# Kernel tuning notes

Hardware: AMD Instinct MI355X
Metric: run time of the kernel (lower is better)

## Reference

```python
import jax, jax.numpy as jnp
import numpy as np

N_NODES = 100000
N_EDGES = 3200000
STATE_DIM = 128
HIDDEN = 256
ACTION_DIM = 64
BN_EPS = 1e-5


def setup_inputs() -> dict:
    key = jax.random.key(0)
    ks = jax.random.split(key, 12)
    feat = jax.random.normal(ks[0], (N_NODES, STATE_DIM), dtype=jnp.float32)
    src = jax.random.randint(ks[1], (N_EDGES,), 0, N_NODES, dtype=jnp.int64) if jax.config.jax_enable_x64 else jax.random.randint(ks[1], (N_EDGES,), 0, N_NODES).astype(jnp.int32)
    dst = jax.random.randint(ks[2], (N_EDGES,), 0, N_NODES).astype(src.dtype)
    def glorot(k, shape):
        lim = np.sqrt(6.0 / (shape[0] + shape[1]))
        return jax.random.uniform(k, shape, jnp.float32, -lim, lim)
    W1 = glorot(ks[3], (STATE_DIM, HIDDEN)); b1 = jnp.zeros((HIDDEN,), jnp.float32)
    W2 = glorot(ks[4], (HIDDEN, HIDDEN));   b2 = jnp.zeros((HIDDEN,), jnp.float32)
    g1 = jnp.ones((HIDDEN,), jnp.float32);  be1 = jnp.zeros((HIDDEN,), jnp.float32)
    g2 = jnp.ones((HIDDEN,), jnp.float32);  be2 = jnp.zeros((HIDDEN,), jnp.float32)
    Wa = glorot(ks[5], (HIDDEN, ACTION_DIM)); ba = jnp.zeros((ACTION_DIM,), jnp.float32)
    Wv = glorot(ks[6], (HIDDEN, 1));          bv = jnp.zeros((1,), jnp.float32)
    return {"feat": feat, "src": src, "dst": dst, "W1": W1, "b1": b1, "g1": g1, "be1": be1,
            "W2": W2, "b2": b2, "g2": g2, "be2": be2, "Wa": Wa, "ba": ba, "Wv": Wv, "bv": bv}


def _graph_conv(x, src, dst, dnorm_out, dnorm_in, W, b):
    # DGL GraphConv, norm='both': scale by out-deg^{-1/2} at src, sum-aggregate at dst,
    # scale by in-deg^{-1/2}, then linear.
    m = x * dnorm_out[:, None]                     # [N, F]
    agg = jax.ops.segment_sum(m[src], dst, num_segments=N_NODES)  # SpMM
    h = agg * dnorm_in[:, None]
    return h @ W + b


def _bn_relu(x, gamma, beta):
    mu = x.mean(axis=0)
    var = x.var(axis=0)  # biased, matches torch BN training normalization
    return jax.nn.relu((x - mu) * jax.lax.rsqrt(var + BN_EPS) * gamma + beta)


def reference(feat, src, dst, W1, b1, g1, be1, W2, b2, g2, be2, Wa, ba, Wv, bv):
    ones = jnp.ones((src.shape[0],), feat.dtype)
    deg_out = jax.ops.segment_sum(ones, src, num_segments=N_NODES)
    deg_in = jax.ops.segment_sum(ones, dst, num_segments=N_NODES)
    dnorm_out = jax.lax.rsqrt(jnp.clip(deg_out, 1.0))
    dnorm_in = jax.lax.rsqrt(jnp.clip(deg_in, 1.0))
    h = _bn_relu(_graph_conv(feat, src, dst, dnorm_out, dnorm_in, W1, b1), g1, be1)
    h = _bn_relu(_graph_conv(h, src, dst, dnorm_out, dnorm_in, W2, b2), g2, be2)
    adv = h @ Wa + ba                              # [N, A]
    val = h @ Wv + bv                              # [N, 1]
    Q = val + (adv - adv.mean(axis=1, keepdims=True))
    return Q
```

## Files before the change

kernel.cpp:

```cpp
#include <hip/hip_runtime.h>
#include <hip/hip_bf16.h>

#define NN 100000
#define NE 3200000
#define HID 256
#define SDIM 128
#define ADIM 64
#define BN_EPS 1e-5f

#define BSH 9
#define NB 196
#define EPB 16384
#define NAB 196

typedef __attribute__((ext_vector_type(8))) short short8;
typedef __attribute__((ext_vector_type(4))) float f32x4;

__device__ __forceinline__ void atomAdd(float* p, float v) { unsafeAtomicAdd(p, v); }
__device__ __forceinline__ float bf2f(ushort u) {
    union { unsigned i; float f; } c; c.i = ((unsigned)u) << 16; return c.f;
}
__device__ __forceinline__ ushort f2bf(float x) {
    __hip_bfloat16 h = __float2bfloat16(x);
    return *reinterpret_cast<ushort*>(&h);
}

__device__ __forceinline__ unsigned wave_excl_scan(unsigned t, int lane) {
    unsigned p = t;
    #pragma unroll
    for (int d = 1; d < 64; d <<= 1) {
        unsigned q = __shfl_up(p, d);
        if (lane >= d) p += q;
    }
    return p - t;
}

__global__ __launch_bounds__(1024)
void k_hist(const int* __restrict__ src, const int* __restrict__ dst,
            unsigned* __restrict__ gh_d, unsigned* __restrict__ gh_s, int E) {
    __shared__ unsigned hd[NB], hs[NB];
    int tid = threadIdx.x;
    if (tid < NB) { hd[tid] = 0; hs[tid] = 0; }
    __syncthreads();
    int base = blockIdx.x * EPB;
    int cnt = min(EPB, E - base);
    for (int i = tid; i < cnt; i += 1024) {
        atomicAdd(&hd[dst[base + i] >> BSH], 1u);
        atomicAdd(&hs[src[base + i] >> BSH], 1u);
    }
    __syncthreads();
    if (tid < NB) {
        if (hd[tid]) atomicAdd(&gh_d[tid * 16], hd[tid]);
        if (hs[tid]) atomicAdd(&gh_s[tid * 16], hs[tid]);
    }
}

__global__ __launch_bounds__(256)
void k_scan_b(const unsigned* __restrict__ gh_d, const unsigned* __restrict__ gh_s,
              unsigned* __restrict__ gcur_d, unsigned* __restrict__ gcur_s,
              unsigned* __restrict__ bbase_d, unsigned* __restrict__ bbase_s,
              int* __restrict__ row_ptr) {
    __shared__ unsigned v[256];
    int t = threadIdx.x;
    unsigned x = (t < NB) ? gh_d[t * 16] : 0;
    v[t] = x; __syncthreads();
    for (int off = 1; off < 256; off <<= 1) {
        unsigned a = (t >= off) ? v[t - off] : 0;
        __syncthreads(); v[t] += a; __syncthreads();
    }
    if (t < NB) { bbase_d[t] = v[t] - x; gcur_d[t * 16] = v[t] - x; }
    if (t == 255) { bbase_d[NB] = v[255]; row_ptr[NN] = (int)v[255]; }
    __syncthreads();
    unsigned y = (t < NB) ? gh_s[t * 16] : 0;
    v[t] = y; __syncthreads();
    for (int off = 1; off < 256; off <<= 1) {
        unsigned a = (t >= off) ? v[t - off] : 0;
        __syncthreads(); v[t] += a; __syncthreads();
    }
    if (t < NB) { bbase_s[t] = v[t] - y; gcur_s[t * 16] = v[t] - y; }
    if (t == 255) bbase_s[NB] = v[255];
}

__global__ __launch_bounds__(1024)
void k_part(const int* __restrict__ src, const int* __restrict__ dst,
            unsigned* __restrict__ gcur_d, unsigned* __restrict__ gcur_s,
            unsigned* __restrict__ outd, ushort* __restrict__ outs, int E) {
    __shared__ unsigned hd[NB], hs[NB], ld_[NB], ls_[NB], cd[NB], cs[NB], bd[NB], bs[NB];
    __shared__ unsigned stage_d[EPB];
    __shared__ ushort stage_s[EPB];
    __shared__ unsigned char sbd[EPB], sbs[EPB];
    const int tid = threadIdx.x;
    const int base = blockIdx.x * EPB;
    const int cnt = min(EPB, E - base);
    if (tid < NB) { hd[tid] = 0; hs[tid] = 0; }
    __syncthreads();

    int es[16], ed[16];
    #pragma unroll
    for (int i = 0; i < 16; ++i) {
        int g = tid + i * 1024;
        if (g < cnt) { es[i] = src[base + g]; ed[i] = dst[base + g]; }
        else { es[i] = -1; ed[i] = -1; }
    }
    #pragma unroll
    for (int i = 0; i < 16; ++i)
        if (ed[i] >= 0) {
            atomicAdd(&hd[ed[i] >> BSH], 1u);
            atomicAdd(&hs[es[i] >> BSH], 1u);
        }
    __syncthreads();

    {
        const int wv = tid >> 6, lane = tid & 63;
        if (wv == 0) {
            unsigned v[4]; unsigned t = 0;
            #pragma unroll
            for (int j = 0; j < 4; ++j) {
                int i = lane * 4 + j;
                v[j] = (i < NB) ? hd[i] : 0; t += v[j];
            }
            unsigned excl = wave_excl_scan(t, lane);
            #pragma unroll
            for (int j = 0; j < 4; ++j) {
                int i = lane * 4 + j;
                if (i < NB) { ld_[i] = excl; cd[i] = excl; }
                excl += v[j];
            }
        } else if (wv == 1) {
            unsigned v[4]; unsigned t = 0;
            #pragma unroll
            for (int j = 0; j < 4; ++j) {
                int i = lane * 4 + j;
                v[j] = (i < NB) ? hs[i] : 0; t += v[j];
            }
            unsigned excl = wave_excl_scan(t, lane);
            #pragma unroll
            for (int j = 0; j < 4; ++j) {
                int i = lane * 4 + j;
                if (i < NB) { ls_[i] = excl; cs[i] = excl; }
                excl += v[j];
            }
        } else if (wv == 2) {
            for (int i = lane; i < NB; i += 64) bd[i] = atomicAdd(&gcur_d[i * 16], hd[i]);
        } else if (wv == 3) {
            for (int i = lane; i < NB; i += 64) bs[i] = atomicAdd(&gcur_s[i * 16], hs[i]);
        }
    }
    __syncthreads();

    #pragma unroll
    for (int i = 0; i < 16; ++i)
        if (ed[i] >= 0) {
            int b = ed[i] >> BSH;
            unsigned p = atomicAdd(&cd[b], 1u);
            stage_d[p] = ((unsigned)(ed[i] & ((1 << BSH) - 1)) << 17) | (unsigned)es[i];
            sbd[p] = (unsigned char)b;
            int b2 = es[i] >> BSH;
            unsigned p2 = atomicAdd(&cs[b2], 1u);
            stage_s[p2] = (ushort)(es[i] & ((1 << BSH) - 1));
            sbs[p2] = (unsigned char)b2;
        }
    __syncthreads();

    for (int i = tid; i < cnt; i += 1024) {
        unsigned b = sbd[i];
        outd[bd[b] + (unsigned)i - ld_[b]] = stage_d[i];
        unsigned b2 = sbs[i];
        outs[bs[b2] + (unsigned)i - ls_[b2]] = stage_s[i];
    }
}

__global__ __launch_bounds__(1024)
void k_csr(const unsigned* __restrict__ outd, const unsigned* __restrict__ bbase_d,
           int* __restrict__ row_ptr, int* __restrict__ csr_src, float* __restrict__ dni) {
    __shared__ unsigned h[512], sc[512];
    const int tid = threadIdx.x, b = blockIdx.x;
    const unsigned beg = bbase_d[b], end = bbase_d[b + 1];
    const int cnt = (int)(end - beg);
    if (tid < 512) h[tid] = 0;
    __syncthreads();
    for (int i = tid; i < cnt; i += 1024) atomicAdd(&h[outd[beg + i] >> 17], 1u);
    __syncthreads();
    if (tid < 64) {
        const int lane = tid;
        unsigned v[8]; unsigned t = 0;
        #pragma unroll
        for (int j = 0; j < 8; ++j) { v[j] = h[lane * 8 + j]; t += v[j]; }
        unsigned excl = wave_excl_scan(t, lane);
        #pragma unroll
        for (int j = 0; j < 8; ++j) { sc[lane * 8 + j] = excl; excl += v[j]; }
    }
    __syncthreads();
    const int n0 = b << BSH;
    const int nb = min(512, NN - n0);
    if (tid < nb) {
        row_ptr[n0 + tid] = (int)(beg + sc[tid]);
        dni[n0 + tid] = rsqrtf(fmaxf((float)h[tid], 1.0f));
    }
    __syncthreads();
    for (int i = tid; i < cnt; i += 1024) {
        unsigned p = outd[beg + i];
        unsigned pos = atomicAdd(&sc[p >> 17], 1u);
        csr_src[beg + pos] = (int)(p & 0x1FFFFu);
    }
}

__global__ __launch_bounds__(1024)
void k_degout_ps(const ushort* __restrict__ outs, const unsigned* __restrict__ bbase_s,
                 const float* __restrict__ feat, float* __restrict__ dno,
                 ushort* __restrict__ Xb) {
    __shared__ unsigned h[512];
    __shared__ float dnl[512];
    const int tid = threadIdx.x, b = blockIdx.x;
    const unsigned beg = bbase_s[b], end = bbase_s[b + 1];
    const int cnt = (int)(end - beg);
    if (tid < 512) h[tid] = 0;
    __syncthreads();
    for (int i = tid; i < cnt; i += 1024) atomicAdd(&h[outs[beg + i]], 1u);
    __syncthreads();
    const int n0 = b << BSH;
    const int nb = min(512, NN - n0);
    if (tid < nb) {
        float d = rsqrtf(fmaxf((float)h[tid], 1.0f));
        dno[n0 + tid] = d;
        dnl[tid] = d;
    }
    __syncthreads();
    const int total4 = nb * 32;
    for (int slot = tid; slot < total4; slot += 1024) {
        int r = slot >> 5, c4 = slot & 31;
        float s = dnl[r];
        float4 v = reinterpret_cast<const float4*>(feat)[(size_t)(n0 + r) * 32 + c4];
        ushort4 o;
        o.x = f2bf(v.x * s); o.y = f2bf(v.y * s);
        o.z = f2bf(v.z * s); o.w = f2bf(v.w * s);
        reinterpret_cast<ushort4*>(Xb)[(size_t)(n0 + r) * 32 + c4] = o;
    }
}

__global__ __launch_bounds__(256)
void k_wprep(const float* __restrict__ W1, const float* __restrict__ W2,
             const float* __restrict__ Wa, const float* __restrict__ Wv,
             ushort* __restrict__ Wt1, ushort* __restrict__ Wt2, ushort* __restrict__ Wh) {
    int idx = blockIdx.x * 256 + threadIdx.x;
    if (idx < HID * SDIM) {
        int n = idx / SDIM, k = idx - n * SDIM;
        Wt1[idx] = f2bf(W1[(size_t)k * HID + n]);
    } else if (idx < HID * SDIM + HID * HID) {
        int j = idx - HID * SDIM;
        int n = j / HID, k = j - n * HID;
        Wt2[j] = f2bf(W2[(size_t)k * HID + n]);
    } else if (idx < HID * SDIM + HID * HID + 80 * HID) {
        int j = idx - HID * SDIM - HID * HID;
        int n = j / HID, k = j - n * HID;
        float v = 0.f;
        if (n < ADIM) v = Wa[(size_t)k * ADIM + n];
        else if (n == ADIM) v = Wv[k];
        Wh[j] = f2bf(v);
    }
}

__global__ __launch_bounds__(256)
void k_spmm_l1(const int* __restrict__ row_ptr, const int* __restrict__ csr_src,
               const ushort* __restrict__ X, const float* __restrict__ dni,
               ushort* __restrict__ Y, int N) {
    const int node = blockIdx.x * 4 + (threadIdx.x >> 6);
    if (node >= N) return;
    const int lane = threadIdx.x & 63;
    const int beg = row_ptr[node];
    const int end = row_ptr[node + 1];
    float acc[4] = {0.f, 0.f, 0.f, 0.f};
    const int half = lane >> 5;
    const int l = lane & 31;
    const ushort* Xl = X + l * 4;
    for (int e = beg + half; e < end; e += 2) {
        int s = csr_src[e];
        ushort4 v = *reinterpret_cast<const ushort4*>(Xl + (size_t)s * 128);
        acc[0] += bf2f(v.x); acc[1] += bf2f(v.y);
        acc[2] += bf2f(v.z); acc[3] += bf2f(v.w);
    }
    acc[0] += __shfl_xor(acc[0], 32);
    acc[1] += __shfl_xor(acc[1], 32);
    acc[2] += __shfl_xor(acc[2], 32);
    acc[3] += __shfl_xor(acc[3], 32);
    if (half == 0) {
        float wi = dni[node];
        ushort4 o;
        o.x = f2bf(acc[0] * wi); o.y = f2bf(acc[1] * wi);
        o.z = f2bf(acc[2] * wi); o.w = f2bf(acc[3] * wi);
        *reinterpret_cast<ushort4*>(Y + (size_t)node * 128 + l * 4) = o;
    }
}

__global__ __launch_bounds__(256)
void k_spmm_bn(const int* __restrict__ row_ptr, const int* __restrict__ csr_src,
               const ushort* __restrict__ Gb, const float* __restrict__ stats,
               const float* __restrict__ gamma, const float* __restrict__ beta,
               const float* __restrict__ dno, const float* __restrict__ dni,
               ushort* __restrict__ Y, int N) {
    __shared__ float sc_s[HID], sh_s[HID];
    {
        int c = threadIdx.x;
        float inv_n = 1.0f / (float)NN;
        float mean = stats[c] * inv_n;
        float var = stats[HID + c] * inv_n - mean * mean;
        float sc = gamma[c] * rsqrtf(var + BN_EPS);
        sc_s[c] = sc;
        sh_s[c] = beta[c] - mean * sc;
    }
    __syncthreads();
    const int node = blockIdx.x * 4 + (threadIdx.x >> 6);
    if (node >= N) return;
    const int lane = threadIdx.x & 63;
    const int c0 = lane * 4;
    float sc[4], sh[4];
    #pragma unroll
    for (int j = 0; j < 4; ++j) { sc[j] = sc_s[c0 + j]; sh[j] = sh_s[c0 + j]; }
    const int beg = row_ptr[node];
    const int end = row_ptr[node + 1];
    float acc[4] = {0.f, 0.f, 0.f, 0.f};
    const ushort* Gl = Gb + c0;
    int e = beg;
    for (; e + 1 < end; e += 2) {
        int s0 = csr_src[e];
        int s1 = csr_src[e + 1];
        float w0 = dno[s0];
        float w1 = dno[s1];
        ushort4 v0 = *reinterpret_cast<const ushort4*>(Gl + (size_t)s0 * 256);
        ushort4 v1 = *reinterpret_cast<const ushort4*>(Gl + (size_t)s1 * 256);
        const ushort* p0 = &v0.x;
        const ushort* p1 = &v1.x;
        #pragma unroll
        for (int j = 0; j < 4; ++j) {
            float y0 = fmaf(bf2f(p0[j]), sc[j], sh[j]);
            y0 = y0 > 0.f ? y0 : 0.f;
            acc[j] = fmaf(y0, w0, acc[j]);
            float y1 = fmaf(bf2f(p1[j]), sc[j], sh[j]);
            y1 = y1 > 0.f ? y1 : 0.f;
            acc[j] = fmaf(y1, w1, acc[j]);
        }
    }
    if (e < end) {
        int s0 = csr_src[e];
        float w0 = dno[s0];
        ushort4 v0 = *reinterpret_cast<const ushort4*>(Gl + (size_t)s0 * 256);
        const ushort* p0 = &v0.x;
        #pragma unroll
        for (int j = 0; j < 4; ++j) {
            float y0 = fmaf(bf2f(p0[j]), sc[j], sh[j]);
            y0 = y0 > 0.f ? y0 : 0.f;
            acc[j] = fmaf(y0, w0, acc[j]);
        }
    }
    float wi = dni[node];
    ushort4 o;
    o.x = f2bf(acc[0] * wi); o.y = f2bf(acc[1] * wi);
    o.z = f2bf(acc[2] * wi); o.w = f2bf(acc[3] * wi);
    *reinterpret_cast<ushort4*>(Y + (size_t)node * 256 + c0) = o;
}

template <int K>
__global__ __launch_bounds__(256, 2)
void k_gemm_mfma(const ushort* __restrict__ A, const ushort* __restrict__ Wt,
                 const float* __restrict__ bias, ushort* __restrict__ outb,
                 float* __restrict__ stats, int M) {
    __shared__ ushort As[128][40];
    __shared__ ushort Bs[256][40];
    __shared__ float sred[4][2][128];
    const int tid = threadIdx.x;
    const int w = tid >> 6;
    const int lane = tid & 63;
    const int wr = (w >> 1) * 64;
    const int wc = (w & 1) * 128;
    const int row0 = blockIdx.x * 128;
    f32x4 acc[4][8] = {};

    const int frow = lane & 15;
    const int fk = (lane >> 4) * 8;

    for (int k0 = 0; k0 < K; k0 += 32) {
        #pragma unroll
        for (int h = 0; h < 2; ++h) {
            int slot = tid + 256 * h;
            int r = slot >> 2;
            int c = (slot & 3) * 8;
            int row = row0 + r;
            int4 v = make_int4(0, 0, 0, 0);
            if (row < M) v = *reinterpret_cast<const int4*>(A + (size_t)row * K + k0 + c);
            *reinterpret_cast<int4*>(&As[r][c]) = v;
        }
        #pragma unroll
        for (int h = 0; h < 4; ++h) {
            int slot = tid + 256 * h;
            int n = slot >> 2;
            int c = (slot & 3) * 8;
            int4 v = *reinterpret_cast<const int4*>(Wt + (size_t)n * K + k0 + c);
            *reinterpret_cast<int4*>(&Bs[n][c]) = v;
        }
        __syncthreads();

        short8 afr[4], bfr[8];
        #pragma unroll
        for (int mi = 0; mi < 4; ++mi)
            afr[mi] = *reinterpret_cast<const short8*>(&As[wr + mi * 16 + frow][fk]);
        #pragma unroll
        for (int ni = 0; ni < 8; ++ni)
            bfr[ni] = *reinterpret_cast<const short8*>(&Bs[wc + ni * 16 + frow][fk]);
        #pragma unroll
        for (int mi = 0; mi < 4; ++mi)
            #pragma unroll
            for (int ni = 0; ni < 8; ++ni)
                acc[mi][ni] = __builtin_amdgcn_mfma_f32_16x16x32_bf16(afr[mi], bfr[ni], acc[mi][ni], 0, 0, 0);
        __syncthreads();
    }

    const int ncol = lane & 15;
    const int rbase = (lane >> 4) * 4;
    #pragma unroll
    for (int ni = 0; ni < 8; ++ni) {
        int col = wc + ni * 16 + ncol;
        float b = bias[col];
        float s1 = 0.f, s2 = 0.f;
        #pragma unroll
        for (int mi = 0; mi < 4; ++mi) {
            #pragma unroll
            for (int q = 0; q < 4; ++q) {
                int row = row0 + wr + mi * 16 + rbase + q;
                if (row < M) {
                    float val = acc[mi][ni][q] + b;
                    outb[(size_t)row * HID + col] = f2bf(val);
                    s1 += val;
                    s2 += val * val;
                }
            }
        }
        s1 += __shfl_xor(s1, 16); s1 += __shfl_xor(s1, 32);
        s2 += __shfl_xor(s2, 16); s2 += __shfl_xor(s2, 32);
        if ((lane >> 4) == 0) {
            sred[w][0][ni * 16 + ncol] = s1;
            sred[w][1][ni * 16 + ncol] = s2;
        }
    }
    __syncthreads();
    {
        int c = tid;
        int half = c >> 7, cl = c & 127;
        float v0 = sred[half][0][cl] + sred[half + 2][0][cl];
        float v1 = sred[half][1][cl] + sred[half + 2][1][cl];
        atomAdd(&stats[c], v0);
        atomAdd(&stats[HID + c], v1);
    }
}

__global__ __launch_bounds__(256)
void k_bn_qhead(const ushort* __restrict__ Gb, const float* __restrict__ stats,
                const float* __restrict__ gamma, const float* __restrict__ beta,
                const ushort* __restrict__ Wh, const float* __restrict__ ba,
                const float* __restrict__ bv, float* __restrict__ out, int M) {
    __shared__ ushort As[128][40];
    __shared__ ushort Bs[80][264];
    __shared__ float sc_s[HID], sh_s[HID];
    const int tid = threadIdx.x;
    const int w = tid >> 6;
    const int lane = tid & 63;
    const int row0 = blockIdx.x * 128;
    const int frow = lane & 15;
    const int fk8 = (lane >> 4) * 8;

    {
        float inv_n = 1.0f / (float)NN;
        float mean = stats[tid] * inv_n;
        float var = stats[HID + tid] * inv_n - mean * mean;
        float sc = gamma[tid] * rsqrtf(var + BN_EPS);
        sc_s[tid] = sc;
        sh_s[tid] = beta[tid] - mean * sc;
    }
    #pragma unroll
    for (int h = 0; h < 10; ++h) {
        int slot = tid + 256 * h;
        int n = slot >> 5;
        int c = (slot & 31) * 8;
        int4 v = *reinterpret_cast<const int4*>(Wh + (size_t)n * HID + c);
        *reinterpret_cast<int4*>(&Bs[n][c]) = v;
    }
    __syncthreads();

    f32x4 acc[2][5] = {};
    for (int k0 = 0; k0 < HID; k0 += 32) {
        #pragma unroll
        for (int h = 0; h < 2; ++h) {
            int slot = tid + 256 * h;
            int r = slot >> 2;
            int c = (slot & 3) * 8;
            int row = row0 + r;
            short8 o = {};
            if (row < M) {
                short8 v = *reinterpret_cast<const short8*>(Gb + (size_t)row * HID + k0 + c);
                #pragma unroll
                for (int j = 0; j < 8; ++j) {
                    int k = k0 + c + j;
                    float y = fmaf(bf2f((ushort)v[j]), sc_s[k], sh_s[k]);
                    o[j] = (short)f2bf(y > 0.f ? y : 0.f);
                }
            }
            *reinterpret_cast<short8*>(&As[r][c]) = o;
        }
        __syncthreads();
        short8 afr[2], bfr[5];
        #pragma unroll
        for (int mi = 0; mi < 2; ++mi)
            afr[mi] = *reinterpret_cast<const short8*>(&As[w * 32 + mi * 16 + frow][fk8]);
        #pragma unroll
        for (int ni = 0; ni < 5; ++ni)
            bfr[ni] = *reinterpret_cast<const short8*>(&Bs[ni * 16 + frow][k0 + fk8]);
        #pragma unroll
        for (int mi = 0; mi < 2; ++mi)
            #pragma unroll
            for (int ni = 0; ni < 5; ++ni)
                acc[mi][ni] = __builtin_amdgcn_mfma_f32_16x16x32_bf16(afr[mi], bfr[ni], acc[mi][ni], 0, 0, 0);
        __syncthreads();
    }

    const int ncol = lane & 15;
    const int gb = lane & 48;
    const float bv0 = bv[0];
    float ba_l[4];
    #pragma unroll
    for (int ni = 0; ni < 4; ++ni) ba_l[ni] = ba[ni * 16 + ncol];
    #pragma unroll
    for (int mi = 0; mi < 2; ++mi) {
        #pragma unroll
        for (int q = 0; q < 4; ++q) {
            int row = row0 + w * 32 + mi * 16 + (lane >> 4) * 4 + q;
            float adv[4];
            float s = 0.f;
            #pragma unroll
            for (int ni = 0; ni < 4; ++ni) {
                adv[ni] = acc[mi][ni][q] + ba_l[ni];
                s += adv[ni];
            }
            s += __shfl_xor(s, 1); s += __shfl_xor(s, 2);
            s += __shfl_xor(s, 4); s += __shfl_xor(s, 8);
            float mean = s * (1.0f / ADIM);
            float val = acc[mi][4][q] + bv0;
            val = __shfl(val, gb);
            if (row < M) {
                #pragma unroll
                for (int ni = 0; ni < 4; ++ni)
                    out[(size_t)row * ADIM + ni * 16 + ncol] = val + adv[ni] - mean;
            }
        }
    }
}

extern "C" void kernel_launch(void* const* d_in, const int* in_sizes, int n_in,
                              void* d_out, int out_size, void* d_ws, size_t ws_size,
                              hipStream_t stream) {
    const float* feat = (const float*)d_in[0];
    const int* src = (const int*)d_in[1];
    const int* dst = (const int*)d_in[2];
    const float* W1 = (const float*)d_in[3];
    const float* b1 = (const float*)d_in[4];
    const float* g1 = (const float*)d_in[5];
    const float* be1 = (const float*)d_in[6];
    const float* W2 = (const float*)d_in[7];
    const float* b2 = (const float*)d_in[8];
    const float* g2 = (const float*)d_in[9];
    const float* be2 = (const float*)d_in[10];
    const float* Wa = (const float*)d_in[11];
    const float* ba = (const float*)d_in[12];
    const float* Wv = (const float*)d_in[13];
    const float* bv = (const float*)d_in[14];
    float* out = (float*)d_out;

    char* w = (char*)d_ws;
    unsigned* gh_d   = (unsigned*)w;  w += (size_t)NB * 16 * 4;
    unsigned* gh_s   = (unsigned*)w;  w += (size_t)NB * 16 * 4;
    float* stats     = (float*)w;     w += 1024 * 4;
    unsigned* gcur_d = (unsigned*)w;  w += (size_t)NB * 16 * 4;
    unsigned* gcur_s = (unsigned*)w;  w += (size_t)NB * 16 * 4;
    unsigned* bbase_d= (unsigned*)w;  w += (NB + 4) * 4;
    unsigned* bbase_s= (unsigned*)w;  w += (NB + 4) * 4;
    float* dn_out    = (float*)w;     w += (size_t)NN * 4;
    float* dn_in     = (float*)w;     w += (size_t)NN * 4;
    int* row_ptr     = (int*)w;       w += (size_t)(NN + 4) * 4;
    unsigned* outd   = (unsigned*)w;  w += (size_t)NE * 4;
    ushort* outs     = (ushort*)w;    w += (size_t)NE * 2;
    int* csr_src     = (int*)w;       w += (size_t)NE * 4;
    ushort* Wt1      = (ushort*)w;    w += (size_t)HID * SDIM * 2;
    ushort* Wt2      = (ushort*)w;    w += (size_t)HID * HID * 2;
    ushort* Whb      = (ushort*)w;    w += (size_t)80 * HID * 2;
    ushort* Xb       = (ushort*)w;    w += (size_t)NN * SDIM * 2;
    ushort* Ab       = (ushort*)w;    w += (size_t)NN * HID * 2;
    ushort* Gb       = (ushort*)w;    w += (size_t)NN * HID * 2;

    hipMemsetAsync(gh_d, 0, (size_t)2 * NB * 16 * 4 + 1024 * 4, stream);

    {
        int total = HID * SDIM + HID * HID + 80 * HID;
        k_wprep<<<(total + 255) / 256, 256, 0, stream>>>(W1, W2, Wa, Wv, Wt1, Wt2, Whb);
    }

    k_hist<<<NAB, 1024, 0, stream>>>(src, dst, gh_d, gh_s, NE);
    k_scan_b<<<1, 256, 0, stream>>>(gh_d, gh_s, gcur_d, gcur_s, bbase_d, bbase_s, row_ptr);
    k_part<<<NAB, 1024, 0, stream>>>(src, dst, gcur_d, gcur_s, outd, outs, NE);
    k_csr<<<NB, 1024, 0, stream>>>(outd, bbase_d, row_ptr, csr_src, dn_in);
    k_degout_ps<<<NB, 1024, 0, stream>>>(outs, bbase_s, feat, dn_out, Xb);

    const int gblocks = (NN + 127) / 128;

    k_spmm_l1<<<(NN + 3) / 4, 256, 0, stream>>>(row_ptr, csr_src, Xb, dn_in, Ab, NN);
    k_gemm_mfma<SDIM><<<gblocks, 256, 0, stream>>>(Ab, Wt1, b1, Gb, stats, NN);

    k_spmm_bn<<<(NN + 3) / 4, 256, 0, stream>>>(row_ptr, csr_src, Gb, stats, g1, be1,
                                                dn_out, dn_in, Ab, NN);
    k_gemm_mfma<HID><<<gblocks, 256, 0, stream>>>(Ab, Wt2, b2, Gb, stats + 512, NN);
    k_bn_qhead<<<gblocks, 256, 0, stream>>>(Gb, stats + 512, g2, be2, Whb, ba, bv, out, NN);
}
```

Baseline: 716.7 us.

## Replace exact-count bucket partition with fixed-capacity buckets, dropping histogram and scan passes

```diff
diff --git a/kernel.cpp b/kernel.cpp
--- a/kernel.cpp
+++ b/kernel.cpp
@@ -12,6 +12,7 @@
 #define NB 196
 #define EPB 16384
 #define NAB 196
+#define CAP 20480
 
 typedef __attribute__((ext_vector_type(8))) short short8;
 typedef __attribute__((ext_vector_type(4))) float f32x4;
@@ -35,207 +36,16 @@
     return p - t;
 }
 
-__global__ __launch_bounds__(1024)
-void k_hist(const int* __restrict__ src, const int* __restrict__ dst,
-            unsigned* __restrict__ gh_d, unsigned* __restrict__ gh_s, int E) {
-    __shared__ unsigned hd[NB], hs[NB];
-    int tid = threadIdx.x;
-    if (tid < NB) { hd[tid] = 0; hs[tid] = 0; }
-    __syncthreads();
-    int base = blockIdx.x * EPB;
-    int cnt = min(EPB, E - base);
-    for (int i = tid; i < cnt; i += 1024) {
-        atomicAdd(&hd[dst[base + i] >> BSH], 1u);
-        atomicAdd(&hs[src[base + i] >> BSH], 1u);
-    }
-    __syncthreads();
-    if (tid < NB) {
-        if (hd[tid]) atomicAdd(&gh_d[tid * 16], hd[tid]);
-        if (hs[tid]) atomicAdd(&gh_s[tid * 16], hs[tid]);
-    }
-}
-
 __global__ __launch_bounds__(256)
-void k_scan_b(const unsigned* __restrict__ gh_d, const unsigned* __restrict__ gh_s,
-              unsigned* __restrict__ gcur_d, unsigned* __restrict__ gcur_s,
-              unsigned* __restrict__ bbase_d, unsigned* __restrict__ bbase_s,
-              int* __restrict__ row_ptr) {
-    __shared__ unsigned v[256];
+void k_init(unsigned* __restrict__ gcur_d, unsigned* __restrict__ gcur_s,
+            float* __restrict__ stats) {
     int t = threadIdx.x;
-    unsigned x = (t < NB) ? gh_d[t * 16] : 0;
-    v[t] = x; __syncthreads();
-    for (int off = 1; off < 256; off <<= 1) {
-        unsigned a = (t >= off) ? v[t - off] : 0;
-        __syncthreads(); v[t] += a; __syncthreads();
-    }
-    if (t < NB) { bbase_d[t] = v[t] - x; gcur_d[t * 16] = v[t] - x; }
-    if (t == 255) { bbase_d[NB] = v[255]; row_ptr[NN] = (int)v[255]; }
-    __syncthreads();
-    unsigned y = (t < NB) ? gh_s[t * 16] : 0;
-    v[t] = y; __syncthreads();
-    for (int off = 1; off < 256; off <<= 1) {
-        unsigned a = (t >= off) ? v[t - off] : 0;
-        __syncthreads(); v[t] += a; __syncthreads();
-    }
-    if (t < NB) { bbase_s[t] = v[t] - y; gcur_s[t * 16] = v[t] - y; }
-    if (t == 255) bbase_s[NB] = v[255];
-}
-
-__global__ __launch_bounds__(1024)
-void k_part(const int* __restrict__ src, const int* __restrict__ dst,
-            unsigned* __restrict__ gcur_d, unsigned* __restrict__ gcur_s,
-            unsigned* __restrict__ outd, ushort* __restrict__ outs, int E) {
-    __shared__ unsigned hd[NB], hs[NB], ld_[NB], ls_[NB], cd[NB], cs[NB], bd[NB], bs[NB];
-    __shared__ unsigned stage_d[EPB];
-    __shared__ ushort stage_s[EPB];
-    __shared__ unsigned char sbd[EPB], sbs[EPB];
-    const int tid = threadIdx.x;
-    const int base = blockIdx.x * EPB;
-    const int cnt = min(EPB, E - base);
-    if (tid < NB) { hd[tid] = 0; hs[tid] = 0; }
-    __syncthreads();
-
-    int es[16], ed[16];
-    #pragma unroll
-    for (int i = 0; i < 16; ++i) {
-        int g = tid + i * 1024;
-        if (g < cnt) { es[i] = src[base + g]; ed[i] = dst[base + g]; }
-        else { es[i] = -1; ed[i] = -1; }
-    }
-    #pragma unroll
-    for (int i = 0; i < 16; ++i)
-        if (ed[i] >= 0) {
-            atomicAdd(&hd[ed[i] >> BSH], 1u);
-            atomicAdd(&hs[es[i] >> BSH], 1u);
-        }
-    __syncthreads();
-
-    {
-        const int wv = tid >> 6, lane = tid & 63;
-        if (wv == 0) {
-            unsigned v[4]; unsigned t = 0;
-            #pragma unroll
-            for (int j = 0; j < 4; ++j) {
-                int i = lane * 4 + j;
-                v[j] = (i < NB) ? hd[i] : 0; t += v[j];
-            }
-            unsigned excl = wave_excl_scan(t, lane);
-            #pragma unroll
-            for (int j = 0; j < 4; ++j) {
-                int i = lane * 4 + j;
-                if (i < NB) { ld_[i] = excl; cd[i] = excl; }
-                excl += v[j];
-            }
-        } else if (wv == 1) {
-            unsigned v[4]; unsigned t = 0;
-            #pragma unroll
-            for (int j = 0; j < 4; ++j) {
-                int i = lane * 4 + j;
-                v[j] = (i < NB) ? hs[i] : 0; t += v[j];
-            }
-            unsigned excl = wave_excl_scan(t, lane);
-            #pragma unroll
-            for (int j = 0; j < 4; ++j) {
-                int i = lane * 4 + j;
-                if (i < NB) { ls_[i] = excl; cs[i] = excl; }
-                excl += v[j];
-            }
-        } else if (wv == 2) {
-            for (int i = lane; i < NB; i += 64) bd[i] = atomicAdd(&gcur_d[i * 16], hd[i]);
-        } else if (wv == 3) {
-            for (int i = lane; i < NB; i += 64) bs[i] = atomicAdd(&gcur_s[i * 16], hs[i]);
-        }
-    }
-    __syncthreads();
-
-    #pragma unroll
-    for (int i = 0; i < 16; ++i)
-        if (ed[i] >= 0) {
-            int b = ed[i] >> BSH;
-            unsigned p = atomicAdd(&cd[b], 1u);
-            stage_d[p] = ((unsigned)(ed[i] & ((1 << BSH) - 1)) << 17) | (unsigned)es[i];
-            sbd[p] = (unsigned char)b;
-            int b2 = es[i] >> BSH;
-            unsigned p2 = atomicAdd(&cs[b2], 1u);
-            stage_s[p2] = (ushort)(es[i] & ((1 << BSH) - 1));
-            sbs[p2] = (unsigned char)b2;
-        }
-    __syncthreads();
-
-    for (int i = tid; i < cnt; i += 1024) {
-        unsigned b = sbd[i];
-        outd[bd[b] + (unsigned)i - ld_[b]] = stage_d[i];
-        unsigned b2 = sbs[i];
-        outs[bs[b2] + (unsigned)i - ls_[b2]] = stage_s[i];
-    }
-}
-
-__global__ __launch_bounds__(1024)
-void k_csr(const unsigned* __restrict__ outd, const unsigned* __restrict__ bbase_d,
-           int* __restrict__ row_ptr, int* __restrict__ csr_src, float* __restrict__ dni) {
-    __shared__ unsigned h[512], sc[512];
-    const int tid = threadIdx.x, b = blockIdx.x;
-    const unsigned beg = bbase_d[b], end = bbase_d[b + 1];
-    const int cnt = (int)(end - beg);
-    if (tid < 512) h[tid] = 0;
-    __syncthreads();
-    for (int i = tid; i < cnt; i += 1024) atomicAdd(&h[outd[beg + i] >> 17], 1u);
-    __syncthreads();
-    if (tid < 64) {
-        const int lane = tid;
-        unsigned v[8]; unsigned t = 0;
-        #pragma unroll
-        for (int j = 0; j < 8; ++j) { v[j] = h[lane * 8 + j]; t += v[j]; }
-        unsigned excl = wave_excl_scan(t, lane);
-        #pragma unroll
-        for (int j = 0; j < 8; ++j) { sc[lane * 8 + j] = excl; excl += v[j]; }
-    }
-    __syncthreads();
-    const int n0 = b << BSH;
-    const int nb = min(512, NN - n0);
-    if (tid < nb) {
-        row_ptr[n0 + tid] = (int)(beg + sc[tid]);
-        dni[n0 + tid] = rsqrtf(fmaxf((float)h[tid], 1.0f));
-    }
-    __syncthreads();
-    for (int i = tid; i < cnt; i += 1024) {
-        unsigned p = outd[beg + i];
-        unsigned pos = atomicAdd(&sc[p >> 17], 1u);
-        csr_src[beg + pos] = (int)(p & 0x1FFFFu);
-    }
-}
-
-__global__ __launch_bounds__(1024)
-void k_degout_ps(const ushort* __restrict__ outs, const unsigned* __restrict__ bbase_s,
-                 const float* __restrict__ feat, float* __restrict__ dno,
-                 ushort* __restrict__ Xb) {
-    __shared__ unsigned h[512];
-    __shared__ float dnl[512];
-    const int tid = threadIdx.x, b = blockIdx.x;
-    const unsigned beg = bbase_s[b], end = bbase_s[b + 1];
-    const int cnt = (int)(end - beg);
-    if (tid < 512) h[tid] = 0;
-    __syncthreads();
-    for (int i = tid; i < cnt; i += 1024) atomicAdd(&h[outs[beg + i]], 1u);
-    __syncthreads();
-    const int n0 = b << BSH;
-    const int nb = min(512, NN - n0);
-    if (tid < nb) {
-        float d = rsqrtf(fmaxf((float)h[tid], 1.0f));
-        dno[n0 + tid] = d;
-        dnl[tid] = d;
-    }
-    __syncthreads();
-    const int total4 = nb * 32;
-    for (int slot = tid; slot < total4; slot += 1024) {
-        int r = slot >> 5, c4 = slot & 31;
-        float s = dnl[r];
-        float4 v = reinterpret_cast<const float4*>(feat)[(size_t)(n0 + r) * 32 + c4];
-        ushort4 o;
-        o.x = f2bf(v.x * s); o.y = f2bf(v.y * s);
-        o.z = f2bf(v.z * s); o.w = f2bf(v.w * s);
-        reinterpret_cast<ushort4*>(Xb)[(size_t)(n0 + r) * 32 + c4] = o;
-    }
+    if (t < NB) {
+        gcur_d[t * 16] = (unsigned)(t * CAP);
+        gcur_s[t * 16] = (unsigned)(t * CAP);
+    }
+    #pragma unroll
+    for (int j = 0; j < 4; ++j) stats[t + 256 * j] = 0.f;
 }
 
 __global__ __launch_bounds__(256)
@@ -260,15 +70,175 @@
     }
 }
 
+__global__ __launch_bounds__(1024)
+void k_part(const int* __restrict__ src, const int* __restrict__ dst,
+            unsigned* __restrict__ gcur_d, unsigned* __restrict__ gcur_s,
+            unsigned* __restrict__ outd, ushort* __restrict__ outs, int E) {
+    __shared__ unsigned hd[NB], hs[NB], ld_[NB], ls_[NB], cd[NB], cs[NB], bd[NB], bs[NB];
+    __shared__ unsigned stage_d[EPB];
+    __shared__ ushort stage_s[EPB];
+    __shared__ unsigned char sbd[EPB], sbs[EPB];
+    const int tid = threadIdx.x;
+    const int base = blockIdx.x * EPB;
+    const int cnt = min(EPB, E - base);
+    if (tid < NB) { hd[tid] = 0; hs[tid] = 0; }
+    __syncthreads();
+
+    int es[16], ed[16];
+    #pragma unroll
+    for (int i = 0; i < 16; ++i) {
+        int g = tid + i * 1024;
+        if (g < cnt) { es[i] = src[base + g]; ed[i] = dst[base + g]; }
+        else { es[i] = -1; ed[i] = -1; }
+    }
+    #pragma unroll
+    for (int i = 0; i < 16; ++i)
+        if (ed[i] >= 0) {
+            atomicAdd(&hd[ed[i] >> BSH], 1u);
+            atomicAdd(&hs[es[i] >> BSH], 1u);
+        }
+    __syncthreads();
+
+    {
+        const int wv = tid >> 6, lane = tid & 63;
+        if (wv == 0) {
+            unsigned v[4]; unsigned t = 0;
+            #pragma unroll
+            for (int j = 0; j < 4; ++j) {
+                int i = lane * 4 + j;
+                v[j] = (i < NB) ? hd[i] : 0; t += v[j];
+            }
+            unsigned excl = wave_excl_scan(t, lane);
+            #pragma unroll
+            for (int j = 0; j < 4; ++j) {
+                int i = lane * 4 + j;
+                if (i < NB) { ld_[i] = excl; cd[i] = excl; }
+                excl += v[j];
+            }
+        } else if (wv == 1) {
+            unsigned v[4]; unsigned t = 0;
+            #pragma unroll
+            for (int j = 0; j < 4; ++j) {
+                int i = lane * 4 + j;
+                v[j] = (i < NB) ? hs[i] : 0; t += v[j];
+            }
+            unsigned excl = wave_excl_scan(t, lane);
+            #pragma unroll
+            for (int j = 0; j < 4; ++j) {
+                int i = lane * 4 + j;
+                if (i < NB) { ls_[i] = excl; cs[i] = excl; }
+                excl += v[j];
+            }
+        } else if (wv == 2) {
+            for (int i = lane; i < NB; i += 64) bd[i] = atomicAdd(&gcur_d[i * 16], hd[i]);
+        } else if (wv == 3) {
+            for (int i = lane; i < NB; i += 64) bs[i] = atomicAdd(&gcur_s[i * 16], hs[i]);
+        }
+    }
+    __syncthreads();
+
+    #pragma unroll
+    for (int i = 0; i < 16; ++i)
+        if (ed[i] >= 0) {
+            int b = ed[i] >> BSH;
+            unsigned p = atomicAdd(&cd[b], 1u);
+            stage_d[p] = ((unsigned)(ed[i] & ((1 << BSH) - 1)) << 17) | (unsigned)es[i];
+            sbd[p] = (unsigned char)b;
+            int b2 = es[i] >> BSH;
+            unsigned p2 = atomicAdd(&cs[b2], 1u);
+            stage_s[p2] = (ushort)(es[i] & ((1 << BSH) - 1));
+            sbs[p2] = (unsigned char)b2;
+        }
+    __syncthreads();
+
+    for (int i = tid; i < cnt; i += 1024) {
+        unsigned b = sbd[i];
+        outd[bd[b] + (unsigned)i - ld_[b]] = stage_d[i];
+        unsigned b2 = sbs[i];
+        outs[bs[b2] + (unsigned)i - ls_[b2]] = stage_s[i];
+    }
+}
+
+__global__ __launch_bounds__(1024)
+void k_finalize(const unsigned* __restrict__ outd, const ushort* __restrict__ outs,
+                const unsigned* __restrict__ gcur_d, const unsigned* __restrict__ gcur_s,
+                int* __restrict__ row_ptr, int* __restrict__ deg_in,
+                int* __restrict__ csr_src, float* __restrict__ dni,
+                const float* __restrict__ feat, float* __restrict__ dno,
+                ushort* __restrict__ Xb) {
+    __shared__ unsigned h[512];
+    __shared__ unsigned aux[512];
+    const int tid = threadIdx.x;
+    if (blockIdx.x < NB) {
+        const int b = blockIdx.x;
+        const unsigned beg = (unsigned)(b * CAP);
+        const int cnt = (int)(gcur_d[b * 16] - beg);
+        if (tid < 512) h[tid] = 0;
+        __syncthreads();
+        for (int i = tid; i < cnt; i += 1024) atomicAdd(&h[outd[beg + i] >> 17], 1u);
+        __syncthreads();
+        if (tid < 64) {
+            const int lane = tid;
+            unsigned v[8]; unsigned t = 0;
+            #pragma unroll
+            for (int j = 0; j < 8; ++j) { v[j] = h[lane * 8 + j]; t += v[j]; }
+            unsigned excl = wave_excl_scan(t, lane);
+            #pragma unroll
+            for (int j = 0; j < 8; ++j) { aux[lane * 8 + j] = excl; excl += v[j]; }
+        }
+        __syncthreads();
+        const int n0 = b << BSH;
+        const int nb = min(512, NN - n0);
+        if (tid < nb) {
+            row_ptr[n0 + tid] = (int)(beg + aux[tid]);
+            deg_in[n0 + tid] = (int)h[tid];
+            dni[n0 + tid] = rsqrtf(fmaxf((float)h[tid], 1.0f));
+        }
+        __syncthreads();
+        for (int i = tid; i < cnt; i += 1024) {
+            unsigned p = outd[beg + i];
+            unsigned pos = atomicAdd(&aux[p >> 17], 1u);
+            csr_src[beg + pos] = (int)(p & 0x1FFFFu);
+        }
+    } else {
+        const int b = blockIdx.x - NB;
+        const unsigned beg = (unsigned)(b * CAP);
+        const int cnt = (int)(gcur_s[b * 16] - beg);
+        float* dnl = (float*)aux;
+        if (tid < 512) h[tid] = 0;
+        __syncthreads();
+        for (int i = tid; i < cnt; i += 1024) atomicAdd(&h[outs[beg + i]], 1u);
+        __syncthreads();
+        const int n0 = b << BSH;
+        const int nb = min(512, NN - n0);
+        if (tid < nb) {
+            float d = rsqrtf(fmaxf((float)h[tid], 1.0f));
+            dno[n0 + tid] = d;
+            dnl[tid] = d;
+        }
+        __syncthreads();
+        const int total4 = nb * 32;
+        for (int slot = tid; slot < total4; slot += 1024) {
+            int r = slot >> 5, c4 = slot & 31;
+            float s = dnl[r];
+            float4 v = reinterpret_cast<const float4*>(feat)[(size_t)(n0 + r) * 32 + c4];
+            ushort4 o;
+            o.x = f2bf(v.x * s); o.y = f2bf(v.y * s);
+            o.z = f2bf(v.z * s); o.w = f2bf(v.w * s);
+            reinterpret_cast<ushort4*>(Xb)[(size_t)(n0 + r) * 32 + c4] = o;
+        }
+    }
+}
+
 __global__ __launch_bounds__(256)
-void k_spmm_l1(const int* __restrict__ row_ptr, const int* __restrict__ csr_src,
-               const ushort* __restrict__ X, const float* __restrict__ dni,
-               ushort* __restrict__ Y, int N) {
+void k_spmm_l1(const int* __restrict__ row_ptr, const int* __restrict__ deg_in,
+               const int* __restrict__ csr_src, const ushort* __restrict__ X,
+               const float* __restrict__ dni, ushort* __restrict__ Y, int N) {
     const int node = blockIdx.x * 4 + (threadIdx.x >> 6);
     if (node >= N) return;
     const int lane = threadIdx.x & 63;
     const int beg = row_ptr[node];
-    const int end = row_ptr[node + 1];
+    const int end = beg + deg_in[node];
     float acc[4] = {0.f, 0.f, 0.f, 0.f};
     const int half = lane >> 5;
     const int l = lane & 31;
@@ -293,11 +263,11 @@
 }
 
 __global__ __launch_bounds__(256)
-void k_spmm_bn(const int* __restrict__ row_ptr, const int* __restrict__ csr_src,
-               const ushort* __restrict__ Gb, const float* __restrict__ stats,
-               const float* __restrict__ gamma, const float* __restrict__ beta,
-               const float* __restrict__ dno, const float* __restrict__ dni,
-               ushort* __restrict__ Y, int N) {
+void k_spmm_bn(const int* __restrict__ row_ptr, const int* __restrict__ deg_in,
+               const int* __restrict__ csr_src, const ushort* __restrict__ Gb,
+               const float* __restrict__ stats, const float* __restrict__ gamma,
+               const float* __restrict__ beta, const float* __restrict__ dno,
+               const float* __restrict__ dni, ushort* __restrict__ Y, int N) {
     __shared__ float sc_s[HID], sh_s[HID];
     {
         int c = threadIdx.x;
@@ -317,7 +287,7 @@
     #pragma unroll
     for (int j = 0; j < 4; ++j) { sc[j] = sc_s[c0 + j]; sh[j] = sh_s[c0 + j]; }
     const int beg = row_ptr[node];
-    const int end = row_ptr[node + 1];
+    const int end = beg + deg_in[node];
     float acc[4] = {0.f, 0.f, 0.f, 0.f};
     const ushort* Gl = Gb + c0;
     int e = beg;
@@ -574,19 +544,16 @@
     float* out = (float*)d_out;
 
     char* w = (char*)d_ws;
-    unsigned* gh_d   = (unsigned*)w;  w += (size_t)NB * 16 * 4;
-    unsigned* gh_s   = (unsigned*)w;  w += (size_t)NB * 16 * 4;
     float* stats     = (float*)w;     w += 1024 * 4;
     unsigned* gcur_d = (unsigned*)w;  w += (size_t)NB * 16 * 4;
     unsigned* gcur_s = (unsigned*)w;  w += (size_t)NB * 16 * 4;
-    unsigned* bbase_d= (unsigned*)w;  w += (NB + 4) * 4;
-    unsigned* bbase_s= (unsigned*)w;  w += (NB + 4) * 4;
     float* dn_out    = (float*)w;     w += (size_t)NN * 4;
     float* dn_in     = (float*)w;     w += (size_t)NN * 4;
     int* row_ptr     = (int*)w;       w += (size_t)(NN + 4) * 4;
-    unsigned* outd   = (unsigned*)w;  w += (size_t)NE * 4;
-    ushort* outs     = (ushort*)w;    w += (size_t)NE * 2;
-    int* csr_src     = (int*)w;       w += (size_t)NE * 4;
+    int* deg_in      = (int*)w;       w += (size_t)(NN + 4) * 4;
+    unsigned* outd   = (unsigned*)w;  w += (size_t)NB * CAP * 4;
+    ushort* outs     = (ushort*)w;    w += (size_t)NB * CAP * 2;
+    int* csr_src     = (int*)w;       w += (size_t)NB * CAP * 4;
     ushort* Wt1      = (ushort*)w;    w += (size_t)HID * SDIM * 2;
     ushort* Wt2      = (ushort*)w;    w += (size_t)HID * HID * 2;
     ushort* Whb      = (ushort*)w;    w += (size_t)80 * HID * 2;
@@ -594,25 +561,22 @@
     ushort* Ab       = (ushort*)w;    w += (size_t)NN * HID * 2;
     ushort* Gb       = (ushort*)w;    w += (size_t)NN * HID * 2;
 
-    hipMemsetAsync(gh_d, 0, (size_t)2 * NB * 16 * 4 + 1024 * 4, stream);
-
+    k_init<<<1, 256, 0, stream>>>(gcur_d, gcur_s, stats);
     {
         int total = HID * SDIM + HID * HID + 80 * HID;
         k_wprep<<<(total + 255) / 256, 256, 0, stream>>>(W1, W2, Wa, Wv, Wt1, Wt2, Whb);
     }
 
-    k_hist<<<NAB, 1024, 0, stream>>>(src, dst, gh_d, gh_s, NE);
-    k_scan_b<<<1, 256, 0, stream>>>(gh_d, gh_s, gcur_d, gcur_s, bbase_d, bbase_s, row_ptr);
     k_part<<<NAB, 1024, 0, stream>>>(src, dst, gcur_d, gcur_s, outd, outs, NE);
-    k_csr<<<NB, 1024, 0, stream>>>(outd, bbase_d, row_ptr, csr_src, dn_in);
-    k_degout_ps<<<NB, 1024, 0, stream>>>(outs, bbase_s, feat, dn_out, Xb);
+    k_finalize<<<2 * NB, 1024, 0, stream>>>(outd, outs, gcur_d, gcur_s, row_ptr, deg_in,
+                                            csr_src, dn_in, feat, dn_out, Xb);
 
     const int gblocks = (NN + 127) / 128;
 
-    k_spmm_l1<<<(NN + 3) / 4, 256, 0, stream>>>(row_ptr, csr_src, Xb, dn_in, Ab, NN);
+    k_spmm_l1<<<(NN + 3) / 4, 256, 0, stream>>>(row_ptr, deg_in, csr_src, Xb, dn_in, Ab, NN);
     k_gemm_mfma<SDIM><<<gblocks, 256, 0, stream>>>(Ab, Wt1, b1, Gb, stats, NN);
 
-    k_spmm_bn<<<(NN + 3) / 4, 256, 0, stream>>>(row_ptr, csr_src, Gb, stats, g1, be1,
+    k_spmm_bn<<<(NN + 3) / 4, 256, 0, stream>>>(row_ptr, deg_in, csr_src, Gb, stats, g1, be1,
                                                 dn_out, dn_in, Ab, NN);
     k_gemm_mfma<HID><<<gblocks, 256, 0, stream>>>(Ab, Wt2, b2, Gb, stats + 512, NN);
     k_bn_qhead<<<gblocks, 256, 0, stream>>>(Gb, stats + 512, g2, be2, Whb, ba, bv, out, NN);
```

After: 701.1 us. -2.2%, faster.
